# Kernel tuning notes

Hardware: AMD Instinct MI355X
Metric: run time of the kernel (lower is better)

The kernel has to match this reference:

```python
import jax, jax.numpy as jnp
import numpy as np

B, N1, N2 = 2, 1024, 1024
D_MODEL, N_HEADS = 2048, 16
HEAD_DIM = D_MODEL // N_HEADS
EPS = 1e-6
ROPE_THETA = 10000.0


def _split_heads(qkv):
    # [b, n, 3*h*d] -> (q, k, v) each [b, h, n, d]
    b, n, _ = qkv.shape
    qkv = qkv.reshape(b, n, 3, N_HEADS, HEAD_DIM)
    qkv = jnp.transpose(qkv, (2, 0, 3, 1, 4))
    return qkv[0], qkv[1], qkv[2]


def _rmsnorm(x, gamma):
    # RMS norm over head dim with learned scale (QKNorm)
    inv = jax.lax.rsqrt(jnp.mean(jnp.square(x), axis=-1, keepdims=True) + EPS)
    return x * inv * gamma


def _rope(x, offset=0):
    # x: [b, h, n, d]; half-split rotary embedding
    n, d = x.shape[-2], x.shape[-1]
    inv_freq = 1.0 / (ROPE_THETA ** (jnp.arange(0, d, 2, dtype=jnp.float32) / d))
    pos = jnp.arange(n, dtype=jnp.float32) + offset
    ang = pos[:, None] * inv_freq  # [n, d/2]
    cos, sin = jnp.cos(ang), jnp.sin(ang)
    x1, x2 = jnp.split(x, 2, axis=-1)
    return jnp.concatenate([x1 * cos - x2 * sin, x1 * sin + x2 * cos], axis=-1)


def _attention(q, k, v):
    # dense path of flex_attention (block_mask=None): softmax(qk^T/sqrt(d)) v
    scale = 1.0 / np.sqrt(HEAD_DIM)
    scores = jnp.einsum('bhqd,bhkd->bhqk', q, k) * scale
    probs = jax.nn.softmax(scores, axis=-1)
    return jnp.einsum('bhqk,bhkd->bhqd', probs, v)


def setup_inputs() -> dict:
    key = jax.random.key(0)
    ks = jax.random.split(key, 8)
    w_std = 0.02
    return {
        'x_1': jax.random.normal(ks[0], (B, N1, D_MODEL), jnp.float32),
        'x_2': jax.random.normal(ks[1], (B, N2, D_MODEL), jnp.float32),
        'w_qkv1': jax.random.normal(ks[2], (D_MODEL, 3 * D_MODEL), jnp.float32) * w_std,
        'b_qkv1': jnp.zeros((3 * D_MODEL,), jnp.float32),
        'w_qkv2': jax.random.normal(ks[3], (D_MODEL, 3 * D_MODEL), jnp.float32) * w_std,
        'b_qkv2': jnp.zeros((3 * D_MODEL,), jnp.float32),
        'qg1': jnp.ones((HEAD_DIM,), jnp.float32),
        'kg1': jnp.ones((HEAD_DIM,), jnp.float32),
        'qg2': jnp.ones((HEAD_DIM,), jnp.float32),
        'kg2': jnp.ones((HEAD_DIM,), jnp.float32),
        'w_out1': jax.random.normal(ks[4], (D_MODEL, D_MODEL), jnp.float32) * w_std,
        'b_out1': jnp.zeros((D_MODEL,), jnp.float32),
        'w_out2': jax.random.normal(ks[5], (D_MODEL, D_MODEL), jnp.float32) * w_std,
        'b_out2': jnp.zeros((D_MODEL,), jnp.float32),
    }


def reference(x_1, x_2, w_qkv1, b_qkv1, w_qkv2, b_qkv2,
              qg1, kg1, qg2, kg2, w_out1, b_out1, w_out2, b_out2):
    n1 = x_1.shape[1]
    qs, ks_, vs = [], [], []
    for x, w, b, qg, kg in ((x_1, w_qkv1, b_qkv1, qg1, kg1),
                            (x_2, w_qkv2, b_qkv2, qg2, kg2)):
        q, k, v = _split_heads(x @ w + b)
        q, k = _rmsnorm(q, qg), _rmsnorm(k, kg)
        qs.append(q); ks_.append(k); vs.append(v)
    q = jnp.concatenate(qs, axis=-2)  # [b, h, n1+n2, d]
    k = jnp.concatenate(ks_, axis=-2)
    v = jnp.concatenate(vs, axis=-2)
    q, k = _rope(q), _rope(k)
    attn = _attention(q, k, v)
    # merge: b h n d -> b n (h d)
    b, h, n, d = attn.shape
    attn = jnp.transpose(attn, (0, 2, 1, 3)).reshape(b, n, h * d)
    out1 = attn[:, :n1] @ w_out1 + b_out1
    out2 = attn[:, n1:] @ w_out2 + b_out2
    return out1, out2
```

## Files before the change

### kernel.cpp

```cpp
#include <hip/hip_runtime.h>

#define DM   2048
#define NH   16
#define HD   128
#define QKVN 6144
#define NTOT 2048

typedef __bf16 bf16x8 __attribute__((ext_vector_type(8)));
typedef float  f32x4  __attribute__((ext_vector_type(4)));
typedef unsigned short ushort_t;

__device__ __forceinline__ unsigned short f2bf(float f) {
  union { float f; unsigned u; } v; v.f = f;
  return (unsigned short)((v.u + 0x7FFFu + ((v.u >> 16) & 1u)) >> 16);
}
__device__ __forceinline__ float bf2f(unsigned short u) {
  union { unsigned u; float f; } v; v.u = ((unsigned)u) << 16;
  return v.f;
}
__device__ __forceinline__ void glds16(const void* g, void* l) {
  __builtin_amdgcn_global_load_lds(
      (const __attribute__((address_space(1))) unsigned int*)g,
      (__attribute__((address_space(3))) unsigned int*)l, 16, 0, 0);
}
#define COMPILER_MEM_BARRIER() asm volatile("" ::: "memory")


__global__ __launch_bounds__(256) void prep_kernel(
    const float* __restrict__ wq1, const float* __restrict__ wq2,
    const float* __restrict__ wo1, const float* __restrict__ wo2,
    const float* __restrict__ x1,  const float* __restrict__ x2,
    ushort_t* __restrict__ wq1t, ushort_t* __restrict__ wq2t,
    ushort_t* __restrict__ wo1t, ushort_t* __restrict__ wo2t,
    ushort_t* __restrict__ xb1,  ushort_t* __restrict__ xb2,
    float2* __restrict__ rtab)
{
  __shared__ __align__(16) unsigned short Ls[64][72];
  const int bid = blockIdx.x, tid = threadIdx.x;
  if (bid < 8192) {
    const float* src; ushort_t* dst; int N, nb, kb;
    if (bid < 6144) {
      src = (bid < 3072) ? wq1 : wq2; dst = (bid < 3072) ? wq1t : wq2t;
      int id = bid % 3072; N = QKVN; nb = id % 96; kb = id / 96;
    } else {
      int id = bid - 6144;
      src = (id < 1024) ? wo1 : wo2; dst = (id < 1024) ? wo1t : wo2t;
      id %= 1024; N = DM; nb = id % 32; kb = id / 32;
    }
    int n0 = nb * 64, k0 = kb * 64;
#pragma unroll
    for (int it = 0; it < 4; ++it) {
      int row = (tid >> 4) + it * 16, c4 = (tid & 15) * 4;
      float4 v = *reinterpret_cast<const float4*>(&src[(size_t)(k0 + row) * N + n0 + c4]);
      Ls[c4 + 0][row] = f2bf(v.x); Ls[c4 + 1][row] = f2bf(v.y);
      Ls[c4 + 2][row] = f2bf(v.z); Ls[c4 + 3][row] = f2bf(v.w);
    }
    __syncthreads();
#pragma unroll
    for (int it = 0; it < 2; ++it) {
      int lin = tid + it * 256, r = lin >> 3, c8 = (lin & 7) * 8;
      *reinterpret_cast<uint4*>(&dst[(size_t)(n0 + r) * 2048 + k0 + c8]) =
          *reinterpret_cast<const uint4*>(&Ls[r][c8]);
    }
  } else if (bid < 10240) {
    int id = bid - 8192;
    const float* src = (id < 1024) ? x1 : x2;
    ushort_t* dst = (id < 1024) ? xb1 : xb2;
    id %= 1024;
    size_t base = (size_t)id * 4096;
#pragma unroll
    for (int it = 0; it < 4; ++it) {
      size_t i = base + (size_t)(it * 256 + tid) * 4;
      float4 v = *reinterpret_cast<const float4*>(&src[i]);
      ushort4 t; t.x = f2bf(v.x); t.y = f2bf(v.y); t.z = f2bf(v.z); t.w = f2bf(v.w);
      *reinterpret_cast<ushort4*>(&dst[i]) = t;
    }
  } else {
    int id = bid - 10240;
    int e0 = id * 16384;
    for (int i = tid; i < 16384; i += 256) {
      int e = e0 + i; int pos = e >> 6, j = e & 63;
      float ang = (float)pos * exp2f(-(float)j * 0.2076205059304601f);
      float s, c; sincosf(ang, &s, &c);
      rtab[e] = make_float2(c, s);
    }
  }
}

__global__ __launch_bounds__(256) void gemm_qkv_f(
    const ushort_t* __restrict__ Xb1, const ushort_t* __restrict__ Xb2,
    const ushort_t* __restrict__ Wt1, const ushort_t* __restrict__ Wt2,
    const float* __restrict__ bq1, const float* __restrict__ bq2,
    const float* __restrict__ qg1, const float* __restrict__ kg1,
    const float* __restrict__ qg2, const float* __restrict__ kg2,
    const float2* __restrict__ rtab,
    ushort_t* __restrict__ Q, ushort_t* __restrict__ K,
    ushort_t* __restrict__ VT)
{
  __shared__ __align__(16) union {
    struct { unsigned short a[8192]; unsigned short b[8192]; } s;
    unsigned short c[128][130];
  } L;
  __shared__ float ssq2[128][2];
  const int z = blockIdx.z;
  const ushort_t* Xb = z ? Xb2 : Xb1;
  const ushort_t* Wt = z ? Wt2 : Wt1;
  const float* bias = z ? bq2 : bq1;
  const float* qg = z ? qg2 : qg1;
  const float* kg = z ? kg2 : kg1;
  const int stream_off = z * 1024;

  const int tid = threadIdx.x, lane = tid & 63, w = tid >> 6;
  const int quad = lane >> 4, l15 = lane & 15;
  const int wrow = (w >> 1) * 64, wcol = (w & 1) * 64;
  const int m0 = blockIdx.y * 128, n0 = blockIdx.x * 128;
  const int lsw = l15 & 7;

  f32x4 acc[4][4];
#pragma unroll
  for (int i = 0; i < 4; i++)
#pragma unroll
    for (int j = 0; j < 4; j++) acc[i][j] = (f32x4){0.f, 0.f, 0.f, 0.f};

  for (int k0 = 0; k0 < DM; k0 += 64) {
#pragma unroll
    for (int it = 0; it < 4; ++it) {
      int c = it * 256 + tid, row = c >> 3, q = (c & 7) ^ (row & 7);
      glds16(&Xb[(size_t)(m0 + row) * 2048 + k0 + q * 8], &L.s.a[c * 8]);
    }
#pragma unroll
    for (int it = 0; it < 4; ++it) {
      int c = it * 256 + tid, row = c >> 3, q = (c & 7) ^ (row & 7);
      glds16(&Wt[(size_t)(n0 + row) * 2048 + k0 + q * 8], &L.s.b[c * 8]);
    }
    __syncthreads();
#pragma unroll
    for (int h = 0; h < 2; ++h) {
      int sq = ((h * 4 + quad) ^ lsw) * 8;
      bf16x8 af[4], bfr[4];
#pragma unroll
      for (int mt = 0; mt < 4; mt++)
        af[mt] = *reinterpret_cast<const bf16x8*>(&L.s.a[(wrow + mt * 16 + l15) * 64 + sq]);
#pragma unroll
      for (int nt = 0; nt < 4; nt++)
        bfr[nt] = *reinterpret_cast<const bf16x8*>(&L.s.b[(wcol + nt * 16 + l15) * 64 + sq]);
#pragma unroll
      for (int mt = 0; mt < 4; mt++)
#pragma unroll
        for (int nt = 0; nt < 4; nt++)
          acc[mt][nt] = __builtin_amdgcn_mfma_f32_16x16x32_bf16(af[mt], bfr[nt], acc[mt][nt], 0, 0, 0);
    }
    __syncthreads();
  }

#pragma unroll
  for (int mt = 0; mt < 4; mt++)
#pragma unroll
    for (int nt = 0; nt < 4; nt++) {
      int col = wcol + nt * 16 + l15;
      float bv = bias[n0 + col];
#pragma unroll
      for (int i = 0; i < 4; i++)
        L.c[wrow + mt * 16 + quad * 4 + i][col] = f2bf(acc[mt][nt][i] + bv);
    }
  __syncthreads();

  const int cc = n0 >> 7, t = cc >> 4, h = cc & 15;
  const int r = tid & 127, half = tid >> 7;
  const int gr = m0 + r, b = gr >> 10;
  const int pos = stream_off + (gr & 1023);
  const int bh = b * NH + h;

  if (t == 2) {
    size_t vb = (size_t)bh * HD * NTOT + pos;
    for (int j = half * 64; j < half * 64 + 64; ++j)
      VT[vb + (size_t)j * NTOT] = L.c[r][j];
  } else {
    float ssq = 0.f;
    for (int j = half * 64; j < half * 64 + 64; ++j) {
      float f = bf2f(L.c[r][j]); ssq += f * f;
    }
    ssq2[r][half] = ssq;
    __syncthreads();
    float inv = rsqrtf((ssq2[r][0] + ssq2[r][1]) * (1.0f / HD) + 1e-6f);
    const float* g = (t == 0) ? qg : kg;
#pragma unroll 4
    for (int jj = 0; jj < 32; ++jj) {
      int j = half * 32 + jj;
      float xv1 = bf2f(L.c[r][j])      * inv * g[j];
      float xv2 = bf2f(L.c[r][j + 64]) * inv * g[j + 64];
      float2 cs = rtab[pos * 64 + j];
      L.c[r][j]      = f2bf(xv1 * cs.x - xv2 * cs.y);
      L.c[r][j + 64] = f2bf(xv1 * cs.y + xv2 * cs.x);
    }
    __syncthreads();
    ushort_t* dst = (t == 0) ? Q : K;
    size_t qb = ((size_t)bh * NTOT + (stream_off + (m0 & 1023))) * HD;
    COMPILER_MEM_BARRIER();
#pragma unroll
    for (int it = 0; it < 32; ++it) {
      int c = it * 256 + tid, rr = c >> 6, cl = c & 63;
      *reinterpret_cast<unsigned int*>(&dst[qb + (size_t)rr * HD + cl * 2]) =
          *reinterpret_cast<const unsigned int*>(&L.c[rr][cl * 2]);
    }
  }
}

__global__ __launch_bounds__(256) void attn_f(
    const ushort_t* __restrict__ Q, const ushort_t* __restrict__ K,
    const ushort_t* __restrict__ VT,
    float* __restrict__ Op, float* __restrict__ Lsum)
{
  __shared__ __align__(16) unsigned short Ks[64 * 128];
  __shared__ __align__(16) unsigned short Vs[128 * 64];
  __shared__ __align__(16) unsigned short Ps[128 * 64];

  const int tid = threadIdx.x, lane = tid & 63, w = tid >> 6;
  const int quad = lane >> 4, l15 = lane & 15;
  const int lsw = l15 & 7;
  const int z = blockIdx.z;
  const int b = z >> 1, split = z & 1;
  const int h = blockIdx.y;
  const int q0 = blockIdx.x * 128;
  const size_t base = (size_t)(b * NH + h) * NTOT * HD;
  const float scale = 0.088388347648318447f;
  const float SHIFT = 16.0f;

  bf16x8 qf[2][4];
#pragma unroll
  for (int mt = 0; mt < 2; mt++)
#pragma unroll
    for (int ks = 0; ks < 4; ks++)
      qf[mt][ks] = *reinterpret_cast<const bf16x8*>(
          &Q[base + (size_t)(q0 + w * 32 + mt * 16 + l15) * HD + ks * 32 + quad * 8]);

  f32x4 oacc[2][8];
#pragma unroll
  for (int mt = 0; mt < 2; mt++)
#pragma unroll
    for (int nt = 0; nt < 8; nt++) oacc[mt][nt] = (f32x4){0.f, 0.f, 0.f, 0.f};
  float lsum[2][4];
#pragma unroll
  for (int mt = 0; mt < 2; mt++)
#pragma unroll
    for (int i = 0; i < 4; i++) lsum[mt][i] = 0.f;

  const int kt0 = split * 16;
  for (int kt = kt0; kt < kt0 + 16; ++kt) {
#pragma unroll
    for (int it = 0; it < 4; ++it) {
      int c = it * 256 + tid, key = c >> 4, q = (c & 15) ^ (key & 15);
      glds16(&K[base + (size_t)(kt * 64 + key) * HD + q * 8], &Ks[c * 8]);
    }
#pragma unroll
    for (int it = 0; it < 4; ++it) {
      int c = it * 256 + tid, d = c >> 3, q = (c & 7) ^ (d & 7);
      glds16(&VT[base + (size_t)d * NTOT + kt * 64 + q * 8], &Vs[c * 8]);
    }
    __syncthreads();

    f32x4 sacc[2][4];
#pragma unroll
    for (int mt = 0; mt < 2; mt++)
#pragma unroll
      for (int nt = 0; nt < 4; nt++) sacc[mt][nt] = (f32x4){0.f, 0.f, 0.f, 0.f};
#pragma unroll
    for (int ks = 0; ks < 4; ks++) {
      bf16x8 kf[4];
#pragma unroll
      for (int nt = 0; nt < 4; nt++)
        kf[nt] = *reinterpret_cast<const bf16x8*>(
            &Ks[(nt * 16 + l15) * 128 + ((ks * 4 + quad) ^ l15) * 8]);
#pragma unroll
      for (int mt = 0; mt < 2; mt++)
#pragma unroll
        for (int nt = 0; nt < 4; nt++)
          sacc[mt][nt] = __builtin_amdgcn_mfma_f32_16x16x32_bf16(qf[mt][ks], kf[nt], sacc[mt][nt], 0, 0, 0);
    }

#pragma unroll
    for (int mt = 0; mt < 2; mt++)
#pragma unroll
      for (int i = 0; i < 4; i++) {
        int rowl = w * 32 + mt * 16 + quad * 4 + i;
        int rb = (quad * 4 + i) & 7;
#pragma unroll
        for (int nt = 0; nt < 4; nt++) {
          float p = __expf(fmaf(sacc[mt][nt][i], scale, -SHIFT));
          lsum[mt][i] += p;
          Ps[rowl * 64 + (((nt * 2 + (l15 >> 3)) ^ rb) * 8) + (l15 & 7)] = f2bf(p);
        }
      }
    COMPILER_MEM_BARRIER();

#pragma unroll
    for (int kk = 0; kk < 2; kk++) {
      bf16x8 pf[2];
#pragma unroll
      for (int mt = 0; mt < 2; mt++)
        pf[mt] = *reinterpret_cast<const bf16x8*>(
            &Ps[(w * 32 + mt * 16 + l15) * 64 + (((kk * 4 + quad) ^ lsw) * 8)]);
#pragma unroll
      for (int nt = 0; nt < 8; nt++) {
        bf16x8 vf = *reinterpret_cast<const bf16x8*>(
            &Vs[(nt * 16 + l15) * 64 + (((kk * 4 + quad) ^ lsw) * 8)]);
#pragma unroll
        for (int mt = 0; mt < 2; mt++)
          oacc[mt][nt] = __builtin_amdgcn_mfma_f32_16x16x32_bf16(pf[mt], vf, oacc[mt][nt], 0, 0, 0);
      }
    }
    __syncthreads();
  }

  const size_t pb = ((size_t)(split * 2 + b) * NH + h) * NTOT;
#pragma unroll
  for (int mt = 0; mt < 2; mt++)
#pragma unroll
    for (int i = 0; i < 4; i++) {
      float l = lsum[mt][i];
      l += __shfl_xor(l, 1); l += __shfl_xor(l, 2);
      l += __shfl_xor(l, 4); l += __shfl_xor(l, 8);
      int qrow = q0 + w * 32 + mt * 16 + quad * 4 + i;
      size_t ob = (pb + qrow) * HD;
#pragma unroll
      for (int nt = 0; nt < 8; nt++)
        Op[ob + nt * 16 + l15] = oacc[mt][nt][i];
      if (l15 == 0) Lsum[pb + qrow] = l;
    }
}

__global__ __launch_bounds__(256) void attn_combine(
    const float* __restrict__ Op, const float* __restrict__ Lsum,
    ushort_t* __restrict__ ATT)
{
  const int tid = threadIdx.x, r = tid >> 4, c8 = (tid & 15) * 8;
  const int row = blockIdx.x * 16 + r;
  const int q = row & 2047, h = (row >> 11) & 15, b = row >> 15;
  const size_t SPLIT = (size_t)2 * NH * NTOT;
  const size_t r0 = ((size_t)b * NH + h) * NTOT + q;
  const size_t r1 = r0 + SPLIT;
  float linv = 1.0f / (Lsum[r0] + Lsum[r1]);
  f32x4 a0 = *reinterpret_cast<const f32x4*>(&Op[r0 * HD + c8]);
  f32x4 a1 = *reinterpret_cast<const f32x4*>(&Op[r0 * HD + c8 + 4]);
  f32x4 b0 = *reinterpret_cast<const f32x4*>(&Op[r1 * HD + c8]);
  f32x4 b1 = *reinterpret_cast<const f32x4*>(&Op[r1 * HD + c8 + 4]);
  ushort_t o[8];
#pragma unroll
  for (int j = 0; j < 4; j++) {
    o[j]     = f2bf((a0[j] + b0[j]) * linv);
    o[j + 4] = f2bf((a1[j] + b1[j]) * linv);
  }
  *reinterpret_cast<uint4*>(&ATT[((size_t)b * NTOT + q) * DM + h * HD + c8]) =
      *reinterpret_cast<const uint4*>(o);
}

__global__ __launch_bounds__(256) void gemm_out_f(
    const ushort_t* __restrict__ A,
    const ushort_t* __restrict__ Wt1, const ushort_t* __restrict__ Wt2,
    const float* __restrict__ bo1, const float* __restrict__ bo2,
    float* __restrict__ Out)
{
  __shared__ __align__(16) unsigned short As[8192];
  __shared__ __align__(16) unsigned short Bs[4096];
  const int z = blockIdx.z;
  const ushort_t* Wt = z ? Wt2 : Wt1;
  const float* bias = z ? bo2 : bo1;
  const int stream_off = z * 1024;
  float* OutZ = Out + (size_t)z * 2 * 1024 * DM;

  const int tid = threadIdx.x, lane = tid & 63, w = tid >> 6;
  const int quad = lane >> 4, l15 = lane & 15;
  const int wrow = (w & 1) * 64, wcol = (w >> 1) * 32;
  const int m0 = blockIdx.y * 128, n0 = blockIdx.x * 64;
  const int lsw = l15 & 7;

  f32x4 acc[4][2];
#pragma unroll
  for (int i = 0; i < 4; i++)
#pragma unroll
    for (int j = 0; j < 2; j++) acc[i][j] = (f32x4){0.f, 0.f, 0.f, 0.f};

  for (int k0 = 0; k0 < DM; k0 += 64) {
#pragma unroll
    for (int it = 0; it < 4; ++it) {
      int c = it * 256 + tid, row = c >> 3, q = (c & 7) ^ (row & 7);
      int gr = m0 + row;
      size_t arow = (size_t)(gr >> 10) * NTOT + stream_off + (gr & 1023);
      glds16(&A[arow * 2048 + k0 + q * 8], &As[c * 8]);
    }
#pragma unroll
    for (int it = 0; it < 2; ++it) {
      int c = it * 256 + tid, row = c >> 3, q = (c & 7) ^ (row & 7);
      glds16(&Wt[(size_t)(n0 + row) * 2048 + k0 + q * 8], &Bs[c * 8]);
    }
    __syncthreads();
#pragma unroll
    for (int h = 0; h < 2; ++h) {
      int sq = ((h * 4 + quad) ^ lsw) * 8;
      bf16x8 af[4], bfr[2];
#pragma unroll
      for (int mt = 0; mt < 4; mt++)
        af[mt] = *reinterpret_cast<const bf16x8*>(&As[(wrow + mt * 16 + l15) * 64 + sq]);
#pragma unroll
      for (int nt = 0; nt < 2; nt++)
        bfr[nt] = *reinterpret_cast<const bf16x8*>(&Bs[(wcol + nt * 16 + l15) * 64 + sq]);
#pragma unroll
      for (int mt = 0; mt < 4; mt++)
#pragma unroll
        for (int nt = 0; nt < 2; nt++)
          acc[mt][nt] = __builtin_amdgcn_mfma_f32_16x16x32_bf16(af[mt], bfr[nt], acc[mt][nt], 0, 0, 0);
    }
    __syncthreads();
  }

#pragma unroll
  for (int mt = 0; mt < 4; mt++)
#pragma unroll
    for (int nt = 0; nt < 2; nt++) {
      int col = n0 + wcol + nt * 16 + l15;
      float bv = bias[col];
#pragma unroll
      for (int i = 0; i < 4; i++) {
        int row = m0 + wrow + mt * 16 + quad * 4 + i;
        OutZ[(size_t)row * DM + col] = acc[mt][nt][i] + bv;
      }
    }
}

union QkvLdsFb {
  struct { unsigned short a[128][40]; unsigned short b[128][40]; } s;
  unsigned short c[128][130];
};

__global__ __launch_bounds__(256) void gemm_qkv_fb(
    const float* __restrict__ X, const float* __restrict__ W,
    const float* __restrict__ bias, const float* __restrict__ qg,
    const float* __restrict__ kg,
    unsigned short* __restrict__ Q, unsigned short* __restrict__ K,
    unsigned short* __restrict__ V, int stream_off)
{
  __shared__ __align__(16) QkvLdsFb L;
  const int tid = threadIdx.x, lane = tid & 63, wv = tid >> 6;
  const int wrow = (wv >> 1) * 64, wcol = (wv & 1) * 64;
  const int quad = lane >> 4, l15 = lane & 15;
  const int m0 = blockIdx.y * 128, n0 = blockIdx.x * 128;
  f32x4 acc[4][4];
#pragma unroll
  for (int i = 0; i < 4; i++)
#pragma unroll
    for (int j = 0; j < 4; j++) acc[i][j] = (f32x4){0.f, 0.f, 0.f, 0.f};
  for (int k0 = 0; k0 < DM; k0 += 32) {
#pragma unroll
    for (int it = 0; it < 4; ++it) {
      int lin = tid + it * 256, row = lin >> 3, c4 = (lin & 7) * 4;
      float4 av = *reinterpret_cast<const float4*>(&X[(size_t)(m0 + row) * DM + k0 + c4]);
      ushort4 t4; t4.x = f2bf(av.x); t4.y = f2bf(av.y); t4.z = f2bf(av.z); t4.w = f2bf(av.w);
      *reinterpret_cast<ushort4*>(&L.s.a[row][c4]) = t4;
    }
#pragma unroll
    for (int it = 0; it < 4; ++it) {
      int lin = tid + it * 256, kr = lin >> 5, c4 = (lin & 31) * 4;
      float4 wv4 = *reinterpret_cast<const float4*>(&W[(size_t)(k0 + kr) * QKVN + n0 + c4]);
      L.s.b[c4 + 0][kr] = f2bf(wv4.x); L.s.b[c4 + 1][kr] = f2bf(wv4.y);
      L.s.b[c4 + 2][kr] = f2bf(wv4.z); L.s.b[c4 + 3][kr] = f2bf(wv4.w);
    }
    __syncthreads();
    bf16x8 af[4], bfr[4];
#pragma unroll
    for (int mt = 0; mt < 4; mt++)
      af[mt] = *reinterpret_cast<const bf16x8*>(&L.s.a[wrow + mt * 16 + l15][quad * 8]);
#pragma unroll
    for (int nt = 0; nt < 4; nt++)
      bfr[nt] = *reinterpret_cast<const bf16x8*>(&L.s.b[wcol + nt * 16 + l15][quad * 8]);
#pragma unroll
    for (int mt = 0; mt < 4; mt++)
#pragma unroll
      for (int nt = 0; nt < 4; nt++)
        acc[mt][nt] = __builtin_amdgcn_mfma_f32_16x16x32_bf16(af[mt], bfr[nt], acc[mt][nt], 0, 0, 0);
    __syncthreads();
  }
#pragma unroll
  for (int mt = 0; mt < 4; mt++)
#pragma unroll
    for (int nt = 0; nt < 4; nt++) {
      int col = wcol + nt * 16 + l15;
      float bv = bias[n0 + col];
#pragma unroll
      for (int i = 0; i < 4; i++)
        L.c[wrow + mt * 16 + quad * 4 + i][col] = f2bf(acc[mt][nt][i] + bv);
    }
  __syncthreads();
  if (tid < 128) {
    int r = tid, cc = n0 >> 7, t = cc >> 4, h = cc & 15;
    int gr = m0 + r, b = gr >> 10, n = gr & 1023, pos = stream_off + n;
    size_t base = ((size_t)(b * NH + h) * NTOT + pos) * HD;
    if (t == 2) {
      for (int j = 0; j < HD; j++) V[base + j] = L.c[r][j];
    } else {
      float ssq = 0.f;
      for (int j = 0; j < HD; j++) { float f = bf2f(L.c[r][j]); ssq += f * f; }
      float inv = rsqrtf(ssq * (1.0f / HD) + 1e-6f);
      const float* g = (t == 0) ? qg : kg;
      unsigned short* dst = (t == 0) ? Q : K;
      for (int j = 0; j < 64; j++) {
        float x1 = bf2f(L.c[r][j]) * inv * g[j];
        float x2 = bf2f(L.c[r][j + 64]) * inv * g[j + 64];
        float ang = (float)pos * exp2f(-(float)j * 0.2076205059304601f);
        float s, c; sincosf(ang, &s, &c);
        dst[base + j] = f2bf(x1 * c - x2 * s);
        dst[base + j + 64] = f2bf(x1 * s + x2 * c);
      }
    }
  }
}

__global__ __launch_bounds__(256) void attn_fb(
    const unsigned short* __restrict__ Q, const unsigned short* __restrict__ K,
    const unsigned short* __restrict__ V, unsigned short* __restrict__ O)
{
  __shared__ __align__(16) unsigned short Ks[64][136];
  __shared__ __align__(16) unsigned short Vt[128][72];
  __shared__ __align__(16) unsigned short Ps[128][72];
  const int tid = threadIdx.x, lane = tid & 63, w = tid >> 6;
  const int quad = lane >> 4, l15 = lane & 15;
  const int b = blockIdx.z, h = blockIdx.y, q0 = blockIdx.x * 128;
  const size_t base = (size_t)(b * NH + h) * NTOT * HD;
  const float scale = 0.088388347648318447f;
  bf16x8 qf[2][4];
#pragma unroll
  for (int mt = 0; mt < 2; mt++)
#pragma unroll
    for (int ks = 0; ks < 4; ks++)
      qf[mt][ks] = *reinterpret_cast<const bf16x8*>(
          &Q[base + (size_t)(q0 + w * 32 + mt * 16 + l15) * HD + ks * 32 + quad * 8]);
  f32x4 oacc[2][8];
#pragma unroll
  for (int mt = 0; mt < 2; mt++)
#pragma unroll
    for (int nt = 0; nt < 8; nt++) oacc[mt][nt] = (f32x4){0.f, 0.f, 0.f, 0.f};
  float mst[2][4], lst[2][4];
#pragma unroll
  for (int mt = 0; mt < 2; mt++)
#pragma unroll
    for (int i = 0; i < 4; i++) { mst[mt][i] = -1e30f; lst[mt][i] = 0.f; }
  for (int kt = 0; kt < NTOT / 64; ++kt) {
#pragma unroll
    for (int it = 0; it < 4; ++it) {
      int lin = tid + it * 256, kr = lin >> 4, c8 = (lin & 15) * 8;
      uint4 kv = *reinterpret_cast<const uint4*>(&K[base + (size_t)(kt * 64 + kr) * HD + c8]);
      *reinterpret_cast<uint4*>(&Ks[kr][c8]) = kv;
      uint4 vv = *reinterpret_cast<const uint4*>(&V[base + (size_t)(kt * 64 + kr) * HD + c8]);
      const unsigned short* vs = reinterpret_cast<const unsigned short*>(&vv);
#pragma unroll
      for (int j = 0; j < 8; j++) Vt[c8 + j][kr] = vs[j];
    }
    __syncthreads();
    f32x4 sacc[2][4];
#pragma unroll
    for (int mt = 0; mt < 2; mt++)
#pragma unroll
      for (int nt = 0; nt < 4; nt++) sacc[mt][nt] = (f32x4){0.f, 0.f, 0.f, 0.f};
#pragma unroll
    for (int ks = 0; ks < 4; ks++) {
      bf16x8 kf[4];
#pragma unroll
      for (int nt = 0; nt < 4; nt++)
        kf[nt] = *reinterpret_cast<const bf16x8*>(&Ks[nt * 16 + l15][ks * 32 + quad * 8]);
#pragma unroll
      for (int mt = 0; mt < 2; mt++)
#pragma unroll
        for (int nt = 0; nt < 4; nt++)
          sacc[mt][nt] = __builtin_amdgcn_mfma_f32_16x16x32_bf16(qf[mt][ks], kf[nt], sacc[mt][nt], 0, 0, 0);
    }
#pragma unroll
    for (int mt = 0; mt < 2; mt++)
#pragma unroll
      for (int i = 0; i < 4; i++) {
        float sv[4]; float rmax = -1e30f;
#pragma unroll
        for (int nt = 0; nt < 4; nt++) { sv[nt] = sacc[mt][nt][i] * scale; rmax = fmaxf(rmax, sv[nt]); }
        rmax = fmaxf(rmax, __shfl_xor(rmax, 1)); rmax = fmaxf(rmax, __shfl_xor(rmax, 2));
        rmax = fmaxf(rmax, __shfl_xor(rmax, 4)); rmax = fmaxf(rmax, __shfl_xor(rmax, 8));
        float mnew = fmaxf(mst[mt][i], rmax);
        float alpha = __expf(mst[mt][i] - mnew);
        float rsum = 0.f;
#pragma unroll
        for (int nt = 0; nt < 4; nt++) {
          float p = __expf(sv[nt] - mnew); rsum += p;
          Ps[w * 32 + mt * 16 + quad * 4 + i][nt * 16 + l15] = f2bf(p);
        }
        rsum += __shfl_xor(rsum, 1); rsum += __shfl_xor(rsum, 2);
        rsum += __shfl_xor(rsum, 4); rsum += __shfl_xor(rsum, 8);
        lst[mt][i] = lst[mt][i] * alpha + rsum; mst[mt][i] = mnew;
#pragma unroll
        for (int nt = 0; nt < 8; nt++) oacc[mt][nt][i] *= alpha;
      }
    __syncthreads();
#pragma unroll
    for (int kk = 0; kk < 2; kk++) {
      bf16x8 pf[2];
#pragma unroll
      for (int mt = 0; mt < 2; mt++)
        pf[mt] = *reinterpret_cast<const bf16x8*>(&Ps[w * 32 + mt * 16 + l15][kk * 32 + quad * 8]);
#pragma unroll
      for (int nt = 0; nt < 8; nt++) {
        bf16x8 vf = *reinterpret_cast<const bf16x8*>(&Vt[nt * 16 + l15][kk * 32 + quad * 8]);
#pragma unroll
        for (int mt = 0; mt < 2; mt++)
          oacc[mt][nt] = __builtin_amdgcn_mfma_f32_16x16x32_bf16(pf[mt], vf, oacc[mt][nt], 0, 0, 0);
      }
    }
    __syncthreads();
  }
#pragma unroll
  for (int mt = 0; mt < 2; mt++)
#pragma unroll
    for (int i = 0; i < 4; i++) {
      float linv = 1.0f / lst[mt][i];
      int qrow = q0 + w * 32 + mt * 16 + quad * 4 + i;
      size_t ob = ((size_t)b * NTOT + qrow) * DM + h * HD;
#pragma unroll
      for (int nt = 0; nt < 8; nt++)
        O[ob + nt * 16 + l15] = f2bf(oacc[mt][nt][i] * linv);
    }
}

__global__ __launch_bounds__(256) void gemm_out_fb(
    const unsigned short* __restrict__ A, const float* __restrict__ W,
    const float* __restrict__ bias, float* __restrict__ Out, int stream_off)
{
  __shared__ __align__(16) struct { unsigned short a[128][40]; unsigned short b[128][40]; } L;
  const int tid = threadIdx.x, lane = tid & 63, wv = tid >> 6;
  const int wrow = (wv >> 1) * 64, wcol = (wv & 1) * 64;
  const int quad = lane >> 4, l15 = lane & 15;
  const int m0 = blockIdx.y * 128, n0 = blockIdx.x * 128;
  f32x4 acc[4][4];
#pragma unroll
  for (int i = 0; i < 4; i++)
#pragma unroll
    for (int j = 0; j < 4; j++) acc[i][j] = (f32x4){0.f, 0.f, 0.f, 0.f};
  for (int k0 = 0; k0 < DM; k0 += 32) {
#pragma unroll
    for (int it = 0; it < 2; ++it) {
      int lin = tid + it * 256, row = lin >> 2, c8 = (lin & 3) * 8;
      int gr = m0 + row, bb = gr >> 10, n = gr & 1023;
      uint4 av = *reinterpret_cast<const uint4*>(
          &A[(size_t)(bb * NTOT + stream_off + n) * DM + k0 + c8]);
      *reinterpret_cast<uint4*>(&L.a[row][c8]) = av;
    }
#pragma unroll
    for (int it = 0; it < 4; ++it) {
      int lin = tid + it * 256, kr = lin >> 5, c4 = (lin & 31) * 4;
      float4 wv4 = *reinterpret_cast<const float4*>(&W[(size_t)(k0 + kr) * DM + n0 + c4]);
      L.b[c4 + 0][kr] = f2bf(wv4.x); L.b[c4 + 1][kr] = f2bf(wv4.y);
      L.b[c4 + 2][kr] = f2bf(wv4.z); L.b[c4 + 3][kr] = f2bf(wv4.w);
    }
    __syncthreads();
    bf16x8 af[4], bfr[4];
#pragma unroll
    for (int mt = 0; mt < 4; mt++)
      af[mt] = *reinterpret_cast<const bf16x8*>(&L.a[wrow + mt * 16 + l15][quad * 8]);
#pragma unroll
    for (int nt = 0; nt < 4; nt++)
      bfr[nt] = *reinterpret_cast<const bf16x8*>(&L.b[wcol + nt * 16 + l15][quad * 8]);
#pragma unroll
    for (int mt = 0; mt < 4; mt++)
#pragma unroll
      for (int nt = 0; nt < 4; nt++)
        acc[mt][nt] = __builtin_amdgcn_mfma_f32_16x16x32_bf16(af[mt], bfr[nt], acc[mt][nt], 0, 0, 0);
    __syncthreads();
  }
#pragma unroll
  for (int mt = 0; mt < 4; mt++)
#pragma unroll
    for (int nt = 0; nt < 4; nt++) {
      int col = wcol + nt * 16 + l15;
      float bv = bias[n0 + col];
#pragma unroll
      for (int i = 0; i < 4; i++) {
        int row = wrow + mt * 16 + quad * 4 + i;
        Out[(size_t)(m0 + row) * DM + n0 + col] = acc[mt][nt][i] + bv;
      }
    }
}

extern "C" void kernel_launch(void* const* d_in, const int* in_sizes, int n_in,
                              void* d_out, int out_size, void* d_ws, size_t ws_size,
                              hipStream_t stream) {
  (void)in_sizes; (void)n_in; (void)out_size;
  const float* x1  = (const float*)d_in[0];
  const float* x2  = (const float*)d_in[1];
  const float* wq1 = (const float*)d_in[2];
  const float* bq1 = (const float*)d_in[3];
  const float* wq2 = (const float*)d_in[4];
  const float* bq2 = (const float*)d_in[5];
  const float* qg1 = (const float*)d_in[6];
  const float* kg1 = (const float*)d_in[7];
  const float* qg2 = (const float*)d_in[8];
  const float* kg2 = (const float*)d_in[9];
  const float* wo1 = (const float*)d_in[10];
  const float* bo1 = (const float*)d_in[11];
  const float* wo2 = (const float*)d_in[12];
  const float* bo2 = (const float*)d_in[13];
  float* out = (float*)d_out;

  unsigned char* wsb = (unsigned char*)d_ws;
  size_t o = 0;
  auto take = [&](size_t bytes) -> void* {
    void* p = wsb + o; o = (o + bytes + 255) & ~(size_t)255; return p;
  };
  ushort_t* Xb1  = (ushort_t*)take((size_t)4194304 * 2);
  ushort_t* Xb2  = (ushort_t*)take((size_t)4194304 * 2);
  ushort_t* Wq1t = (ushort_t*)take((size_t)12582912 * 2);
  ushort_t* Wq2t = (ushort_t*)take((size_t)12582912 * 2);
  ushort_t* Wo1t = (ushort_t*)take((size_t)4194304 * 2);
  ushort_t* Wo2t = (ushort_t*)take((size_t)4194304 * 2);
  float2*   rtab = (float2*)take((size_t)131072 * 8);
  ushort_t* Qf   = (ushort_t*)take((size_t)8388608 * 2);
  ushort_t* Kf   = (ushort_t*)take((size_t)8388608 * 2);
  ushort_t* VTf  = (ushort_t*)take((size_t)8388608 * 2);
  ushort_t* ATTf = (ushort_t*)take((size_t)8388608 * 2);
  const size_t need = o;
  float* Op   = (float*)Xb1;
  float* Lsum = (float*)rtab;

  dim3 blk(256);
  if (ws_size >= need) {
    hipLaunchKernelGGL(prep_kernel, dim3(10248), blk, 0, stream,
                       wq1, wq2, wo1, wo2, x1, x2,
                       Wq1t, Wq2t, Wo1t, Wo2t, Xb1, Xb2, rtab);
    hipLaunchKernelGGL(gemm_qkv_f, dim3(48, 16, 2), blk, 0, stream,
                       Xb1, Xb2, Wq1t, Wq2t, bq1, bq2, qg1, kg1, qg2, kg2,
                       rtab, Qf, Kf, VTf);
    hipLaunchKernelGGL(attn_f, dim3(16, 16, 4), blk, 0, stream, Qf, Kf, VTf, Op, Lsum);
    hipLaunchKernelGGL(attn_combine, dim3(4096), blk, 0, stream, Op, Lsum, ATTf);
    hipLaunchKernelGGL(gemm_out_f, dim3(32, 16, 2), blk, 0, stream,
                       ATTf, Wo1t, Wo2t, bo1, bo2, out);
  } else {
    const size_t QKV_ELEMS = (size_t)2 * NH * NTOT * HD;
    unsigned short* Q   = (unsigned short*)d_ws;
    unsigned short* K   = Q + QKV_ELEMS;
    unsigned short* V   = K + QKV_ELEMS;
    unsigned short* ATT = V + QKV_ELEMS;
    hipLaunchKernelGGL(gemm_qkv_fb, dim3(48, 16), blk, 0, stream, x1, wq1, bq1, qg1, kg1, Q, K, V, 0);
    hipLaunchKernelGGL(gemm_qkv_fb, dim3(48, 16), blk, 0, stream, x2, wq2, bq2, qg2, kg2, Q, K, V, 1024);
    hipLaunchKernelGGL(attn_fb, dim3(16, 16, 2), blk, 0, stream, Q, K, V, ATT);
    hipLaunchKernelGGL(gemm_out_fb, dim3(16, 16), blk, 0, stream, ATT, wo1, bo1, out, 0);
    hipLaunchKernelGGL(gemm_out_fb, dim3(16, 16), blk, 0, stream,
                       ATT, wo2, bo2, out + (size_t)2 * 1024 * DM, 1024);
  }
}
```

Before: 502.4 us.

## Vectorize V-transpose stores and alias P buffer onto K tile in attention

The QKV epilogue for the V third now writes the transposed V with 16-byte vector stores of 8 consecutive positions per column, replacing per-element scalar strided stores. The attention kernel drops the separate P shared buffer and reuses the K tile's shared memory for P, adding a barrier after the QK^T MMAs so no wave overwrites K while others still read it. Launch bounds request 4 blocks per SM. This cuts LDS use per block to raise occupancy, at the cost of one extra barrier per key tile and possible register pressure from the occupancy hint.

```diff
diff --git a/kernel.cpp b/kernel.cpp
--- a/kernel.cpp
+++ b/kernel.cpp
@@ -166,16 +166,25 @@
   __syncthreads();
 
   const int cc = n0 >> 7, t = cc >> 4, h = cc & 15;
-  const int r = tid & 127, half = tid >> 7;
-  const int gr = m0 + r, b = gr >> 10;
-  const int pos = stream_off + (gr & 1023);
-  const int bh = b * NH + h;
+  const int bq = m0 >> 10;
+  const int pos0 = stream_off + (m0 & 1023);
+  const int bh = bq * NH + h;
 
   if (t == 2) {
-    size_t vb = (size_t)bh * HD * NTOT + pos;
-    for (int j = half * 64; j < half * 64 + 64; ++j)
-      VT[vb + (size_t)j * NTOT] = L.c[r][j];
+    size_t vb = (size_t)bh * HD * NTOT;
+#pragma unroll
+    for (int it = 0; it < 8; ++it) {
+      int task = it * 256 + tid;
+      int j = task & 127, g = task >> 7;
+      ushort_t tmp[8];
+#pragma unroll
+      for (int s = 0; s < 8; ++s) tmp[s] = L.c[g * 8 + s][j];
+      *reinterpret_cast<uint4*>(&VT[vb + (size_t)j * NTOT + pos0 + g * 8]) =
+          *reinterpret_cast<const uint4*>(tmp);
+    }
   } else {
+    const int r = tid & 127, half = tid >> 7;
+    const int pos = pos0 + r;
     float ssq = 0.f;
     for (int j = half * 64; j < half * 64 + 64; ++j) {
       float f = bf2f(L.c[r][j]); ssq += f * f;
@@ -195,7 +204,7 @@
     }
     __syncthreads();
     ushort_t* dst = (t == 0) ? Q : K;
-    size_t qb = ((size_t)bh * NTOT + (stream_off + (m0 & 1023))) * HD;
+    size_t qb = ((size_t)bh * NTOT + pos0) * HD;
     COMPILER_MEM_BARRIER();
 #pragma unroll
     for (int it = 0; it < 32; ++it) {
@@ -206,14 +215,13 @@
   }
 }
 
-__global__ __launch_bounds__(256) void attn_f(
+__global__ __launch_bounds__(256, 4) void attn_f(
     const ushort_t* __restrict__ Q, const ushort_t* __restrict__ K,
     const ushort_t* __restrict__ VT,
     float* __restrict__ Op, float* __restrict__ Lsum)
 {
-  __shared__ __align__(16) unsigned short Ks[64 * 128];
+  __shared__ __align__(16) unsigned short KP[64 * 128];
   __shared__ __align__(16) unsigned short Vs[128 * 64];
-  __shared__ __align__(16) unsigned short Ps[128 * 64];
 
   const int tid = threadIdx.x, lane = tid & 63, w = tid >> 6;
   const int quad = lane >> 4, l15 = lane & 15;
@@ -250,7 +258,7 @@
 #pragma unroll
     for (int it = 0; it < 4; ++it) {
       int c = it * 256 + tid, key = c >> 4, q = (c & 15) ^ (key & 15);
-      glds16(&K[base + (size_t)(kt * 64 + key) * HD + q * 8], &Ks[c * 8]);
+      glds16(&K[base + (size_t)(kt * 64 + key) * HD + q * 8], &KP[c * 8]);
     }
 #pragma unroll
     for (int it = 0; it < 4; ++it) {
@@ -270,13 +278,14 @@
 #pragma unroll
       for (int nt = 0; nt < 4; nt++)
         kf[nt] = *reinterpret_cast<const bf16x8*>(
-            &Ks[(nt * 16 + l15) * 128 + ((ks * 4 + quad) ^ l15) * 8]);
+            &KP[(nt * 16 + l15) * 128 + ((ks * 4 + quad) ^ l15) * 8]);
 #pragma unroll
       for (int mt = 0; mt < 2; mt++)
 #pragma unroll
         for (int nt = 0; nt < 4; nt++)
           sacc[mt][nt] = __builtin_amdgcn_mfma_f32_16x16x32_bf16(qf[mt][ks], kf[nt], sacc[mt][nt], 0, 0, 0);
     }
+    __syncthreads();
 
 #pragma unroll
     for (int mt = 0; mt < 2; mt++)
@@ -288,7 +297,7 @@
         for (int nt = 0; nt < 4; nt++) {
           float p = __expf(fmaf(sacc[mt][nt][i], scale, -SHIFT));
           lsum[mt][i] += p;
-          Ps[rowl * 64 + (((nt * 2 + (l15 >> 3)) ^ rb) * 8) + (l15 & 7)] = f2bf(p);
+          KP[rowl * 64 + (((nt * 2 + (l15 >> 3)) ^ rb) * 8) + (l15 & 7)] = f2bf(p);
         }
       }
     COMPILER_MEM_BARRIER();
@@ -299,7 +308,7 @@
 #pragma unroll
       for (int mt = 0; mt < 2; mt++)
         pf[mt] = *reinterpret_cast<const bf16x8*>(
-            &Ps[(w * 32 + mt * 16 + l15) * 64 + (((kk * 4 + quad) ^ lsw) * 8)]);
+            &KP[(w * 32 + mt * 16 + l15) * 64 + (((kk * 4 + quad) ^ lsw) * 8)]);
 #pragma unroll
       for (int nt = 0; nt < 8; nt++) {
         bf16x8 vf = *reinterpret_cast<const bf16x8*>(
```

Result: slower. 707.4 us (+40.8%).
